# Kernel optimization log

Measured on AMD Instinct MI355X. Metric: run time of the kernel, lower is better.

Reference implementation:

```python
import jax, jax.numpy as jnp
import numpy as np

B, L, D, H = 2, 4096, 768, 12
Dh = D // H


def setup_inputs() -> dict:
    key = jax.random.key(0)
    k1, k2, k3 = jax.random.split(key, 3)
    x = jax.random.normal(k1, (B, L, D), dtype=jnp.float32)
    Wqkv = jax.random.normal(k2, (D, 3 * D), dtype=jnp.float32) * 0.02
    bqkv = jnp.zeros((3 * D,), dtype=jnp.float32)
    Wo = jax.random.normal(k3, (D, D), dtype=jnp.float32) * 0.02
    bo = jnp.zeros((D,), dtype=jnp.float32)
    return {"x": x, "Wqkv": Wqkv, "bqkv": bqkv, "Wo": Wo, "bo": bo}


def reference(x, Wqkv, bqkv, Wo, bo):
    Bs, Ls, Ds = x.shape
    # fused QKV projection
    qkv = x @ Wqkv + bqkv  # [B, L, 3D]
    q, k, v = jnp.split(qkv, 3, axis=2)
    q = q.reshape(Bs, Ls, H, Dh)
    k = k.reshape(Bs, Ls, H, Dh)
    v = v.reshape(Bs, Ls, H, Dh)
    # scaled dot-product attention with causal mask (fp32 softmax, as flax dpa with dtype=float32)
    scale = 1.0 / np.sqrt(Dh)
    scores = jnp.einsum('bqhd,bkhd->bhqk', q, k) * scale  # [B, H, L, L]
    causal = jnp.tril(jnp.ones((Ls, Ls), dtype=bool))
    big_neg = jnp.finfo(jnp.float32).min
    scores = jnp.where(causal[None, None, :, :], scores, big_neg)
    attn = jax.nn.softmax(scores, axis=-1)
    y = jnp.einsum('bhqk,bkhd->bqhd', attn, v)  # [B, L, H, Dh]
    y = y.reshape(Bs, Ls, Ds)
    # output projection
    return y @ Wo + bo
```

## Files before the change

kernel.cpp:

```cpp
#include <hip/hip_runtime.h>
#include <hip/hip_bf16.h>
#include <stdint.h>

#define BB 2
#define LL 4096
#define DD 768
#define HH 12
#define DH 64
#define MM (BB * LL)
#define NQKV (3 * DD)
#define KK 768
#define PLANE ((size_t)BB * HH * LL * DH)
#define SQSCALE 0.1803368801111204f

typedef __attribute__((ext_vector_type(8))) short bf16x8;
typedef __attribute__((ext_vector_type(4))) float f32x4;

__device__ __forceinline__ float bf2f(uint16_t u) {
  union { uint32_t u; float f; } c; c.u = ((uint32_t)u) << 16; return c.f;
}
__device__ __forceinline__ uint16_t f2bf(float f) {
  union { float f; uint32_t u; } c; c.f = f;
  return (uint16_t)((c.u + 0x7FFFu + ((c.u >> 16) & 1u)) >> 16);
}
__device__ __forceinline__ uint32_t cvt2(float a, float b) {
  __hip_bfloat162 h = __float22bfloat162_rn(make_float2(a, b));
  union { __hip_bfloat162 h; uint32_t u; } c; c.h = h; return c.u;
}

union H8 { uint16_t h[8]; uint32_t w[4]; uint4 v; };
union B8 { uint2 d[2]; bf16x8 v; };

template <bool F32>
__device__ __forceinline__ H8 load8(const void* p, size_t idx) {
  H8 r;
  if (F32) {
    const float* f = (const float*)p + idx;
    float4 a = *(const float4*)f;
    float4 b = *(const float4*)(f + 4);
    r.w[0] = cvt2(a.x, a.y); r.w[1] = cvt2(a.z, a.w);
    r.w[2] = cvt2(b.x, b.y); r.w[3] = cvt2(b.z, b.w);
  } else {
    r.v = *(const uint4*)((const uint16_t*)p + idx);
  }
  return r;
}

__device__ __forceinline__ void g2l16(const uint16_t* g, uint16_t* l) {
  __builtin_amdgcn_global_load_lds((const __attribute__((address_space(1))) void*)g,
                                   (__attribute__((address_space(3))) void*)l,
                                   16, 0, 0);
}

__global__ void detect_k(const uint16_t* __restrict__ x, int* __restrict__ flag) {
  __shared__ int cnt;
  if (threadIdx.x == 0) cnt = 0;
  __syncthreads();
  int c = 0;
  for (int i = threadIdx.x; i < 4096; i += 256) {
    int e = (x[i] >> 7) & 0xFF;
    if (e == 0xFF || e > 133 || e < 100) c++;
  }
  atomicAdd(&cnt, c);
  __syncthreads();
  if (threadIdx.x == 0) *flag = (cnt > 512) ? 1 : 0;
}

__global__ __launch_bounds__(256) void prep_k(const void* __restrict__ x,
                                              uint16_t* __restrict__ xbf,
                                              const void* __restrict__ Wqkv,
                                              uint16_t* __restrict__ wqkvT,
                                              const void* __restrict__ Wo,
                                              uint16_t* __restrict__ woT,
                                              const int* __restrict__ flag) {
  __shared__ uint16_t Ts[64][65];
  const int fl = *flag;
  const int id = blockIdx.x;
  const int tid = threadIdx.x;
  if (id < 768) {
    size_t base = (size_t)id * 1024 + tid;
#pragma unroll
    for (int j = 0; j < 4; ++j) {
      size_t i = base + j * 256;
      H8 v = fl ? load8<true>(x, i * 8) : load8<false>(x, i * 8);
      *(uint4*)(xbf + i * 8) = v.v;
    }
    return;
  }
  const void* W;
  uint16_t* WT;
  int N, widx;
  if (id < 1200) { W = Wqkv; WT = wqkvT; N = NQKV; widx = id - 768; }
  else           { W = Wo;   WT = woT;   N = DD;   widx = id - 1200; }
  const int nb = N / 64;
  const int n0 = (widx % nb) * 64, k0 = (widx / nb) * 64;
#pragma unroll
  for (int j = 0; j < 16; ++j) {
    int idx = tid + j * 256;
    int r = idx >> 6, c = idx & 63;
    size_t gi = (size_t)(k0 + r) * N + n0 + c;
    float v = fl ? ((const float*)W)[gi] : bf2f(((const uint16_t*)W)[gi]);
    Ts[c][r] = f2bf(v);
  }
  __syncthreads();
#pragma unroll
  for (int j = 0; j < 16; ++j) {
    int idx = tid + j * 256;
    int n = idx >> 6, k = idx & 63;
    WT[(size_t)(n0 + n) * KK + k0 + k] = Ts[n][k];
  }
}

__device__ __forceinline__ void gemm128_core(const uint16_t* __restrict__ A,
                                             const uint16_t* __restrict__ BT,
                                             int m0, int n0,
                                             uint16_t* As, uint16_t* Bs,
                                             f32x4 acc[4][4]) {
  const int tid = threadIdx.x, lane = tid & 63, w = tid >> 6;
  const int quad = lane >> 4, c16 = lane & 15;
  const int wm = w >> 1, wn = w & 1;
  const int srow = lane >> 2, schunk = lane & 3;
  const int rsw = (c16 >> 1) & 3;
  for (int k0 = 0; k0 < KK; k0 += 32) {
#pragma unroll
    for (int i = 0; i < 2; ++i) {
      int row = w * 32 + i * 16 + srow;
      int gch = schunk ^ ((row >> 1) & 3);
      g2l16(A + (size_t)(m0 + row) * KK + k0 + gch * 8, As + (w * 32 + i * 16) * 32);
      g2l16(BT + (size_t)(n0 + row) * KK + k0 + gch * 8, Bs + (w * 32 + i * 16) * 32);
    }
    __syncthreads();
    bf16x8 a[4], b[4];
#pragma unroll
    for (int i = 0; i < 4; ++i) {
      a[i] = *(const bf16x8*)(As + (wm * 64 + i * 16 + c16) * 32 + ((quad ^ rsw) * 8));
      b[i] = *(const bf16x8*)(Bs + (wn * 64 + i * 16 + c16) * 32 + ((quad ^ rsw) * 8));
    }
#pragma unroll
    for (int i = 0; i < 4; ++i)
#pragma unroll
      for (int f = 0; f < 4; ++f)
        acc[i][f] = __builtin_amdgcn_mfma_f32_16x16x32_bf16(a[i], b[f], acc[i][f], 0, 0, 0);
    __syncthreads();
  }
}

__global__ __launch_bounds__(256) void qkv128_k(const uint16_t* __restrict__ X,
                                                const uint16_t* __restrict__ WT,
                                                const void* __restrict__ bias,
                                                uint16_t* __restrict__ planes,
                                                const int* __restrict__ flag) {
  __shared__ __align__(16) uint16_t smem[8704];
  uint16_t* As = smem;
  uint16_t* Bs = smem + 4096;
  const int fl = *flag;
  const int m0 = blockIdx.x * 128, n0 = blockIdx.y * 128;
  f32x4 acc[4][4];
#pragma unroll
  for (int i = 0; i < 4; ++i)
#pragma unroll
    for (int f = 0; f < 4; ++f) acc[i][f] = (f32x4){0.f, 0.f, 0.f, 0.f};
  gemm128_core(X, WT, m0, n0, As, Bs, acc);

  const int tid = threadIdx.x, lane = tid & 63, w = tid >> 6;
  const int quad = lane >> 4, c16 = lane & 15;
  const int wm = w >> 1, wn = w & 1;
  const int which = (n0 >= 2 * DD) ? 2 : (n0 >= DD ? 1 : 0);

  if (which < 2) {
    uint16_t* dst = planes + (size_t)which * PLANE;
    const float sc = (which == 0) ? SQSCALE : 1.0f;
#pragma unroll
    for (int f = 0; f < 4; ++f) {
      int n = n0 + wn * 64 + f * 16 + c16;
      float bv = fl ? ((const float*)bias)[n] : bf2f(((const uint16_t*)bias)[n]);
      int rem = n - which * DD;
      int hh = rem >> 6, dd = rem & 63;
#pragma unroll
      for (int i = 0; i < 4; ++i) {
        uint32_t pa = cvt2((acc[i][f][0] + bv) * sc, (acc[i][f][1] + bv) * sc);
        uint32_t pb = cvt2((acc[i][f][2] + bv) * sc, (acc[i][f][3] + bv) * sc);
        int m = m0 + wm * 64 + i * 16 + quad * 4;
        int b = m >> 12, l = m & (LL - 1);
        uint16_t* base = dst + ((size_t)(b * HH + hh) * LL + l) * DH + dd;
        base[0 * DH] = (uint16_t)pa;
        base[1 * DH] = (uint16_t)(pa >> 16);
        base[2 * DH] = (uint16_t)pb;
        base[3 * DH] = (uint16_t)(pb >> 16);
      }
    }
  } else {
    uint16_t (*Ts)[136] = reinterpret_cast<uint16_t(*)[136]>(smem);
    uint16_t* vtp = planes + 2 * PLANE;
    const int l0 = m0 & (LL - 1), bb = m0 >> 12;
    for (int half = 0; half < 2; ++half) {
      __syncthreads();
      if (wn == half) {
#pragma unroll
        for (int f = 0; f < 4; ++f) {
          int n = n0 + half * 64 + f * 16 + c16;
          float bv = fl ? ((const float*)bias)[n] : bf2f(((const uint16_t*)bias)[n]);
#pragma unroll
          for (int i = 0; i < 4; ++i) {
            uint32_t pa = cvt2(acc[i][f][0] + bv, acc[i][f][1] + bv);
            uint32_t pb = cvt2(acc[i][f][2] + bv, acc[i][f][3] + bv);
            *(uint2*)(&Ts[f * 16 + c16][wm * 64 + i * 16 + quad * 4]) = make_uint2(pa, pb);
          }
        }
      }
      __syncthreads();
#pragma unroll
      for (int j = 0; j < 4; ++j) {
        int idx = tid + j * 256;
        int nl = idx >> 4, ch = idx & 15;
        int rem = n0 + half * 64 + nl - 2 * DD;
        int hh = rem >> 6, dd = rem & 63;
        uint4 val = *(const uint4*)(&Ts[nl][ch * 8]);
        *(uint4*)(vtp + ((size_t)(bb * HH + hh) * DH + dd) * LL + l0 + ch * 8) = val;
      }
    }
  }
}

__global__ __launch_bounds__(256) void attn_k(const uint16_t* __restrict__ planes,
                                              uint16_t* __restrict__ y) {
  __shared__ __align__(16) uint16_t Ks[2][64 * 64];
  __shared__ __align__(16) uint16_t Vt[2][64 * 64];
  __shared__ __align__(16) uint16_t Ps[4][16 * 64];
  const int p = blockIdx.x;
  const int bh = blockIdx.y;
  const uint16_t* qb = planes + (size_t)bh * LL * DH;
  const uint16_t* kb = qb + PLANE;
  const uint16_t* vtb = planes + 2 * PLANE + (size_t)bh * DH * LL;
  const int tid = threadIdx.x, lane = tid & 63, wv = tid >> 6;
  const int quad = lane >> 4, c16 = lane & 15;
  const int r0 = tid >> 3, c0 = tid & 7;
  const int sw0 = r0 & 7;
  const int swf = c16 & 7;
  uint16_t* Psb = Ps[wv];
  const int b = bh / HH, hh = bh - b * HH;
  const int pwbase = c16 * 64;
  const int prd0 = pwbase + (((2 * quad) ^ c16) << 2);
  const int prd1 = pwbase + (((2 * quad + 1) ^ c16) << 2);
  const int prd2 = pwbase + (((8 + 2 * quad) ^ c16) << 2);
  const int prd3 = pwbase + (((8 + 2 * quad + 1) ^ c16) << 2);

  for (int pass = 0; pass < 2; ++pass) {
    const int qi = pass ? p : 63 - p;
    const int q0 = qi * 64;
    const size_t qoff = (size_t)(q0 + wv * 16 + c16) * DH;
    bf16x8 qf0 = *(const bf16x8*)(qb + qoff + quad * 8);
    bf16x8 qf1 = *(const bf16x8*)(qb + qoff + 32 + quad * 8);

    f32x4 o[4];
#pragma unroll
    for (int g = 0; g < 4; ++g) o[g] = (f32x4){0.f, 0.f, 0.f, 0.f};
    float l_i = 0.f;

    uint4 kr0 = *(const uint4*)(kb + (size_t)r0 * DH + c0 * 8);
    uint4 kr1 = *(const uint4*)(kb + (size_t)(r0 + 32) * DH + c0 * 8);
    uint4 vr0 = *(const uint4*)(vtb + (size_t)r0 * LL + c0 * 8);
    uint4 vr1 = *(const uint4*)(vtb + (size_t)(r0 + 32) * LL + c0 * 8);

    for (int t = 0; t <= qi; ++t) {
      uint16_t* kd = Ks[t & 1];
      uint16_t* vd = Vt[t & 1];
      *(uint4*)(kd + r0 * 64 + (c0 ^ sw0) * 8) = kr0;
      *(uint4*)(kd + (r0 + 32) * 64 + (c0 ^ sw0) * 8) = kr1;
      *(uint4*)(vd + r0 * 64 + (c0 ^ sw0) * 8) = vr0;
      *(uint4*)(vd + (r0 + 32) * 64 + (c0 ^ sw0) * 8) = vr1;
      if (t < qi) {
        int t64 = (t + 1) * 64;
        kr0 = *(const uint4*)(kb + (size_t)(t64 + r0) * DH + c0 * 8);
        kr1 = *(const uint4*)(kb + (size_t)(t64 + r0 + 32) * DH + c0 * 8);
        vr0 = *(const uint4*)(vtb + (size_t)r0 * LL + t64 + c0 * 8);
        vr1 = *(const uint4*)(vtb + (size_t)(r0 + 32) * LL + t64 + c0 * 8);
      }
      __syncthreads();

      f32x4 s[4];
#pragma unroll
      for (int f = 0; f < 4; ++f) {
        const uint16_t* krow = kd + (f * 16 + c16) * 64;
        bf16x8 k0f = *(const bf16x8*)(krow + ((quad ^ swf) * 8));
        bf16x8 k1f = *(const bf16x8*)(krow + (((quad + 4) ^ swf) * 8));
        f32x4 z = {0.f, 0.f, 0.f, 0.f};
        z = __builtin_amdgcn_mfma_f32_16x16x32_bf16(k0f, qf0, z, 0, 0, 0);
        z = __builtin_amdgcn_mfma_f32_16x16x32_bf16(k1f, qf1, z, 0, 0, 0);
        s[f] = z;
      }
      const int qg = q0 + wv * 16 + c16;
      if (t == qi) {
#pragma unroll
        for (int f = 0; f < 4; ++f) {
          int key0 = t * 64 + f * 16 + quad * 4;
#pragma unroll
          for (int r = 0; r < 4; ++r) {
            float pv = exp2f(s[f][r]);
            pv = (key0 + r <= qg) ? pv : 0.f;
            s[f][r] = pv;
            l_i += pv;
          }
        }
      } else {
#pragma unroll
        for (int f = 0; f < 4; ++f)
#pragma unroll
          for (int r = 0; r < 4; ++r) {
            float pv = exp2f(s[f][r]);
            s[f][r] = pv;
            l_i += pv;
          }
      }
#pragma unroll
      for (int f = 0; f < 4; ++f) {
        uint32_t w0 = cvt2(s[f][0], s[f][1]);
        uint32_t w1 = cvt2(s[f][2], s[f][3]);
        *(uint2*)(Psb + pwbase + (((f * 4 + quad) ^ c16) << 2)) = make_uint2(w0, w1);
      }
      __asm__ __volatile__("s_waitcnt lgkmcnt(0)" ::: "memory");
      B8 p0, p1;
      p0.d[0] = *(const uint2*)(Psb + prd0);
      p0.d[1] = *(const uint2*)(Psb + prd1);
      p1.d[0] = *(const uint2*)(Psb + prd2);
      p1.d[1] = *(const uint2*)(Psb + prd3);
#pragma unroll
      for (int g = 0; g < 4; ++g) {
        const uint16_t* vrow = vd + (g * 16 + c16) * 64;
        bf16x8 v0 = *(const bf16x8*)(vrow + ((quad ^ swf) * 8));
        bf16x8 v1 = *(const bf16x8*)(vrow + (((quad + 4) ^ swf) * 8));
        o[g] = __builtin_amdgcn_mfma_f32_16x16x32_bf16(p0.v, v0, o[g], 0, 0, 0);
        o[g] = __builtin_amdgcn_mfma_f32_16x16x32_bf16(p1.v, v1, o[g], 0, 0, 0);
      }
    }

    l_i += __shfl_xor(l_i, 16);
    l_i += __shfl_xor(l_i, 32);
    float inv[4];
#pragma unroll
    for (int r = 0; r < 4; ++r)
      inv[r] = 1.f / __shfl(l_i, (quad << 4) + quad * 4 + r);
#pragma unroll
    for (int g = 0; g < 4; ++g) {
      uint32_t pa = cvt2(o[g][0] * inv[0], o[g][1] * inv[1]);
      uint32_t pb = cvt2(o[g][2] * inv[2], o[g][3] * inv[3]);
      int l = q0 + wv * 16 + quad * 4;
      uint16_t* base = y + ((size_t)(b * LL + l)) * DD + hh * DH + g * 16 + c16;
      base[0 * DD] = (uint16_t)pa;
      base[1 * DD] = (uint16_t)(pa >> 16);
      base[2 * DD] = (uint16_t)pb;
      base[3 * DD] = (uint16_t)(pb >> 16);
    }
    __syncthreads();
  }
}

__global__ __launch_bounds__(256) void out64_k(const uint16_t* __restrict__ Y,
                                               const uint16_t* __restrict__ WT,
                                               const void* __restrict__ bias,
                                               void* __restrict__ out,
                                               const int* __restrict__ flag) {
  __shared__ __align__(16) uint16_t As[128 * 32];
  __shared__ __align__(16) uint16_t Bs[64 * 32];
  const int fl = *flag;
  const int m0 = blockIdx.x * 128, n0 = blockIdx.y * 64;
  const int tid = threadIdx.x, lane = tid & 63, w = tid >> 6;
  const int quad = lane >> 4, c16 = lane & 15;
  const int srow = lane >> 2, schunk = lane & 3;
  const int rsw = (c16 >> 1) & 3;
  f32x4 acc[2][4];
#pragma unroll
  for (int i = 0; i < 2; ++i)
#pragma unroll
    for (int f = 0; f < 4; ++f) acc[i][f] = (f32x4){0.f, 0.f, 0.f, 0.f};
  for (int k0 = 0; k0 < KK; k0 += 32) {
#pragma unroll
    for (int i = 0; i < 2; ++i) {
      int row = w * 32 + i * 16 + srow;
      int gch = schunk ^ ((row >> 1) & 3);
      g2l16(Y + (size_t)(m0 + row) * KK + k0 + gch * 8, As + (w * 32 + i * 16) * 32);
    }
    {
      int row = w * 16 + srow;
      int gch = schunk ^ ((row >> 1) & 3);
      g2l16(WT + (size_t)(n0 + row) * KK + k0 + gch * 8, Bs + (w * 16) * 32);
    }
    __syncthreads();
    bf16x8 a[2], bfr[4];
#pragma unroll
    for (int i = 0; i < 2; ++i)
      a[i] = *(const bf16x8*)(As + (w * 32 + i * 16 + c16) * 32 + ((quad ^ rsw) * 8));
#pragma unroll
    for (int f = 0; f < 4; ++f)
      bfr[f] = *(const bf16x8*)(Bs + (f * 16 + c16) * 32 + ((quad ^ rsw) * 8));
#pragma unroll
    for (int i = 0; i < 2; ++i)
#pragma unroll
      for (int f = 0; f < 4; ++f)
        acc[i][f] = __builtin_amdgcn_mfma_f32_16x16x32_bf16(a[i], bfr[f], acc[i][f], 0, 0, 0);
    __syncthreads();
  }
#pragma unroll
  for (int f = 0; f < 4; ++f) {
    int n = n0 + f * 16 + c16;
    float bv = fl ? ((const float*)bias)[n] : bf2f(((const uint16_t*)bias)[n]);
#pragma unroll
    for (int i = 0; i < 2; ++i) {
      int m = m0 + w * 32 + i * 16 + quad * 4;
      if (fl) {
        float* base = (float*)out + (size_t)m * DD + n;
#pragma unroll
        for (int r = 0; r < 4; ++r) base[r * DD] = acc[i][f][r] + bv;
      } else {
        uint32_t pa = cvt2(acc[i][f][0] + bv, acc[i][f][1] + bv);
        uint32_t pb = cvt2(acc[i][f][2] + bv, acc[i][f][3] + bv);
        uint16_t* base = (uint16_t*)out + (size_t)m * DD + n;
        base[0 * DD] = (uint16_t)pa;
        base[1 * DD] = (uint16_t)(pa >> 16);
        base[2 * DD] = (uint16_t)pb;
        base[3 * DD] = (uint16_t)(pb >> 16);
      }
    }
  }
}

extern "C" void kernel_launch(void* const* d_in, const int* in_sizes, int n_in,
                              void* d_out, int out_size, void* d_ws, size_t ws_size,
                              hipStream_t stream) {
  const void* x    = d_in[0];
  const void* Wqkv = d_in[1];
  const void* bqkv = d_in[2];
  const void* Wo   = d_in[3];
  const void* bo   = d_in[4];
  int* flagp = (int*)d_ws;
  uint16_t* planes = (uint16_t*)((char*)d_ws + 64);
  uint16_t* y_ws   = planes + 3 * PLANE;
  uint16_t* wqkvT  = y_ws + (size_t)MM * DD;
  uint16_t* woT    = wqkvT + (size_t)NQKV * KK;
  uint16_t* xbf    = y_ws;

  detect_k<<<1, 256, 0, stream>>>((const uint16_t*)x, flagp);
  prep_k<<<1344, 256, 0, stream>>>(x, xbf, Wqkv, wqkvT, Wo, woT, flagp);
  qkv128_k<<<dim3(MM / 128, NQKV / 128), 256, 0, stream>>>(xbf, wqkvT, bqkv, planes, flagp);
  attn_k<<<dim3(32, BB * HH), 256, 0, stream>>>(planes, y_ws);
  out64_k<<<dim3(MM / 128, DD / 64), 256, 0, stream>>>(y_ws, woT, bo, d_out, flagp);
}
```

Baseline: 272.4 us.

## Feed P from registers via permuted V layout and launch one q-tile per block

```diff
diff --git a/kernel.cpp b/kernel.cpp
--- a/kernel.cpp
+++ b/kernel.cpp
@@ -226,8 +226,7 @@
                                               uint16_t* __restrict__ y) {
   __shared__ __align__(16) uint16_t Ks[2][64 * 64];
   __shared__ __align__(16) uint16_t Vt[2][64 * 64];
-  __shared__ __align__(16) uint16_t Ps[4][16 * 64];
-  const int p = blockIdx.x;
+  const int qi = 63 - blockIdx.x;
   const int bh = blockIdx.y;
   const uint16_t* qb = planes + (size_t)bh * LL * DH;
   const uint16_t* kb = qb + PLANE;
@@ -237,121 +236,122 @@
   const int r0 = tid >> 3, c0 = tid & 7;
   const int sw0 = r0 & 7;
   const int swf = c16 & 7;
-  uint16_t* Psb = Ps[wv];
   const int b = bh / HH, hh = bh - b * HH;
-  const int pwbase = c16 * 64;
-  const int prd0 = pwbase + (((2 * quad) ^ c16) << 2);
-  const int prd1 = pwbase + (((2 * quad + 1) ^ c16) << 2);
-  const int prd2 = pwbase + (((8 + 2 * quad) ^ c16) << 2);
-  const int prd3 = pwbase + (((8 + 2 * quad + 1) ^ c16) << 2);
-
-  for (int pass = 0; pass < 2; ++pass) {
-    const int qi = pass ? p : 63 - p;
-    const int q0 = qi * 64;
-    const size_t qoff = (size_t)(q0 + wv * 16 + c16) * DH;
-    bf16x8 qf0 = *(const bf16x8*)(qb + qoff + quad * 8);
-    bf16x8 qf1 = *(const bf16x8*)(qb + qoff + 32 + quad * 8);
-
-    f32x4 o[4];
-#pragma unroll
-    for (int g = 0; g < 4; ++g) o[g] = (f32x4){0.f, 0.f, 0.f, 0.f};
-    float l_i = 0.f;
-
-    uint4 kr0 = *(const uint4*)(kb + (size_t)r0 * DH + c0 * 8);
-    uint4 kr1 = *(const uint4*)(kb + (size_t)(r0 + 32) * DH + c0 * 8);
-    uint4 vr0 = *(const uint4*)(vtb + (size_t)r0 * LL + c0 * 8);
-    uint4 vr1 = *(const uint4*)(vtb + (size_t)(r0 + 32) * LL + c0 * 8);
-
-    for (int t = 0; t <= qi; ++t) {
-      uint16_t* kd = Ks[t & 1];
-      uint16_t* vd = Vt[t & 1];
-      *(uint4*)(kd + r0 * 64 + (c0 ^ sw0) * 8) = kr0;
-      *(uint4*)(kd + (r0 + 32) * 64 + (c0 ^ sw0) * 8) = kr1;
-      *(uint4*)(vd + r0 * 64 + (c0 ^ sw0) * 8) = vr0;
-      *(uint4*)(vd + (r0 + 32) * 64 + (c0 ^ sw0) * 8) = vr1;
-      if (t < qi) {
-        int t64 = (t + 1) * 64;
-        kr0 = *(const uint4*)(kb + (size_t)(t64 + r0) * DH + c0 * 8);
-        kr1 = *(const uint4*)(kb + (size_t)(t64 + r0 + 32) * DH + c0 * 8);
-        vr0 = *(const uint4*)(vtb + (size_t)r0 * LL + t64 + c0 * 8);
-        vr1 = *(const uint4*)(vtb + (size_t)(r0 + 32) * LL + t64 + c0 * 8);
+
+  const int kw0 = r0 * 64 + (c0 ^ sw0) * 8;
+  const int kw1 = (r0 + 32) * 64 + (c0 ^ sw0) * 8;
+  int vw0, vw1, vw2, vw3;
+  {
+    int ksA = 8 * c0;
+    int ksB = 8 * c0 + 4;
+    int chA = ((ksA & 32) >> 3) + ((ksA >> 2) & 3);
+    int chB = ((ksB & 32) >> 3) + ((ksB >> 2) & 3);
+    int fA = ((ksA >> 4) & 1) * 4;
+    int fB = ((ksB >> 4) & 1) * 4;
+    vw0 = r0 * 64 + ((chA ^ sw0) * 8) + fA;
+    vw1 = r0 * 64 + ((chB ^ sw0) * 8) + fB;
+    vw2 = (r0 + 32) * 64 + ((chA ^ sw0) * 8) + fA;
+    vw3 = (r0 + 32) * 64 + ((chB ^ sw0) * 8) + fB;
+  }
+
+  const int q0 = qi * 64;
+  const size_t qoff = (size_t)(q0 + wv * 16 + c16) * DH;
+  bf16x8 qf0 = *(const bf16x8*)(qb + qoff + quad * 8);
+  bf16x8 qf1 = *(const bf16x8*)(qb + qoff + 32 + quad * 8);
+
+  f32x4 o[4];
+#pragma unroll
+  for (int g = 0; g < 4; ++g) o[g] = (f32x4){0.f, 0.f, 0.f, 0.f};
+  float l_i = 0.f;
+
+  uint4 kr0 = *(const uint4*)(kb + (size_t)r0 * DH + c0 * 8);
+  uint4 kr1 = *(const uint4*)(kb + (size_t)(r0 + 32) * DH + c0 * 8);
+  uint4 vr0 = *(const uint4*)(vtb + (size_t)r0 * LL + c0 * 8);
+  uint4 vr1 = *(const uint4*)(vtb + (size_t)(r0 + 32) * LL + c0 * 8);
+
+  for (int t = 0; t <= qi; ++t) {
+    uint16_t* kd = Ks[t & 1];
+    uint16_t* vd = Vt[t & 1];
+    *(uint4*)(kd + kw0) = kr0;
+    *(uint4*)(kd + kw1) = kr1;
+    *(uint2*)(vd + vw0) = make_uint2(vr0.x, vr0.y);
+    *(uint2*)(vd + vw1) = make_uint2(vr0.z, vr0.w);
+    *(uint2*)(vd + vw2) = make_uint2(vr1.x, vr1.y);
+    *(uint2*)(vd + vw3) = make_uint2(vr1.z, vr1.w);
+    if (t < qi) {
+      int t64 = (t + 1) * 64;
+      kr0 = *(const uint4*)(kb + (size_t)(t64 + r0) * DH + c0 * 8);
+      kr1 = *(const uint4*)(kb + (size_t)(t64 + r0 + 32) * DH + c0 * 8);
+      vr0 = *(const uint4*)(vtb + (size_t)r0 * LL + t64 + c0 * 8);
+      vr1 = *(const uint4*)(vtb + (size_t)(r0 + 32) * LL + t64 + c0 * 8);
+    }
+    __syncthreads();
+
+    f32x4 s[4];
+#pragma unroll
+    for (int f = 0; f < 4; ++f) {
+      const uint16_t* krow = kd + (f * 16 + c16) * 64;
+      bf16x8 k0f = *(const bf16x8*)(krow + ((quad ^ swf) * 8));
+      bf16x8 k1f = *(const bf16x8*)(krow + (((quad + 4) ^ swf) * 8));
+      f32x4 z = {0.f, 0.f, 0.f, 0.f};
+      z = __builtin_amdgcn_mfma_f32_16x16x32_bf16(k0f, qf0, z, 0, 0, 0);
+      z = __builtin_amdgcn_mfma_f32_16x16x32_bf16(k1f, qf1, z, 0, 0, 0);
+      s[f] = z;
+    }
+    const int qg = q0 + wv * 16 + c16;
+    if (t == qi) {
+#pragma unroll
+      for (int f = 0; f < 4; ++f) {
+        int key0 = t * 64 + f * 16 + quad * 4;
+#pragma unroll
+        for (int r = 0; r < 4; ++r) {
+          float pv = exp2f(s[f][r]);
+          pv = (key0 + r <= qg) ? pv : 0.f;
+          s[f][r] = pv;
+          l_i += pv;
+        }
       }
-      __syncthreads();
-
-      f32x4 s[4];
-#pragma unroll
-      for (int f = 0; f < 4; ++f) {
-        const uint16_t* krow = kd + (f * 16 + c16) * 64;
-        bf16x8 k0f = *(const bf16x8*)(krow + ((quad ^ swf) * 8));
-        bf16x8 k1f = *(const bf16x8*)(krow + (((quad + 4) ^ swf) * 8));
-        f32x4 z = {0.f, 0.f, 0.f, 0.f};
-        z = __builtin_amdgcn_mfma_f32_16x16x32_bf16(k0f, qf0, z, 0, 0, 0);
-        z = __builtin_amdgcn_mfma_f32_16x16x32_bf16(k1f, qf1, z, 0, 0, 0);
-        s[f] = z;
-      }
-      const int qg = q0 + wv * 16 + c16;
-      if (t == qi) {
-#pragma unroll
-        for (int f = 0; f < 4; ++f) {
-          int key0 = t * 64 + f * 16 + quad * 4;
-#pragma unroll
-          for (int r = 0; r < 4; ++r) {
-            float pv = exp2f(s[f][r]);
-            pv = (key0 + r <= qg) ? pv : 0.f;
-            s[f][r] = pv;
-            l_i += pv;
-          }
+    } else {
+#pragma unroll
+      for (int f = 0; f < 4; ++f)
+#pragma unroll
+        for (int r = 0; r < 4; ++r) {
+          float pv = exp2f(s[f][r]);
+          s[f][r] = pv;
+          l_i += pv;
         }
-      } else {
-#pragma unroll
-        for (int f = 0; f < 4; ++f)
-#pragma unroll
-          for (int r = 0; r < 4; ++r) {
-            float pv = exp2f(s[f][r]);
-            s[f][r] = pv;
-            l_i += pv;
-          }
-      }
-#pragma unroll
-      for (int f = 0; f < 4; ++f) {
-        uint32_t w0 = cvt2(s[f][0], s[f][1]);
-        uint32_t w1 = cvt2(s[f][2], s[f][3]);
-        *(uint2*)(Psb + pwbase + (((f * 4 + quad) ^ c16) << 2)) = make_uint2(w0, w1);
-      }
-      __asm__ __volatile__("s_waitcnt lgkmcnt(0)" ::: "memory");
-      B8 p0, p1;
-      p0.d[0] = *(const uint2*)(Psb + prd0);
-      p0.d[1] = *(const uint2*)(Psb + prd1);
-      p1.d[0] = *(const uint2*)(Psb + prd2);
-      p1.d[1] = *(const uint2*)(Psb + prd3);
-#pragma unroll
-      for (int g = 0; g < 4; ++g) {
-        const uint16_t* vrow = vd + (g * 16 + c16) * 64;
-        bf16x8 v0 = *(const bf16x8*)(vrow + ((quad ^ swf) * 8));
-        bf16x8 v1 = *(const bf16x8*)(vrow + (((quad + 4) ^ swf) * 8));
-        o[g] = __builtin_amdgcn_mfma_f32_16x16x32_bf16(p0.v, v0, o[g], 0, 0, 0);
-        o[g] = __builtin_amdgcn_mfma_f32_16x16x32_bf16(p1.v, v1, o[g], 0, 0, 0);
-      }
-    }
-
-    l_i += __shfl_xor(l_i, 16);
-    l_i += __shfl_xor(l_i, 32);
-    float inv[4];
-#pragma unroll
-    for (int r = 0; r < 4; ++r)
-      inv[r] = 1.f / __shfl(l_i, (quad << 4) + quad * 4 + r);
+    }
+    B8 p0, p1;
+    p0.d[0] = make_uint2(cvt2(s[0][0], s[0][1]), cvt2(s[0][2], s[0][3]));
+    p0.d[1] = make_uint2(cvt2(s[1][0], s[1][1]), cvt2(s[1][2], s[1][3]));
+    p1.d[0] = make_uint2(cvt2(s[2][0], s[2][1]), cvt2(s[2][2], s[2][3]));
+    p1.d[1] = make_uint2(cvt2(s[3][0], s[3][1]), cvt2(s[3][2], s[3][3]));
 #pragma unroll
     for (int g = 0; g < 4; ++g) {
-      uint32_t pa = cvt2(o[g][0] * inv[0], o[g][1] * inv[1]);
-      uint32_t pb = cvt2(o[g][2] * inv[2], o[g][3] * inv[3]);
-      int l = q0 + wv * 16 + quad * 4;
-      uint16_t* base = y + ((size_t)(b * LL + l)) * DD + hh * DH + g * 16 + c16;
-      base[0 * DD] = (uint16_t)pa;
-      base[1 * DD] = (uint16_t)(pa >> 16);
-      base[2 * DD] = (uint16_t)pb;
-      base[3 * DD] = (uint16_t)(pb >> 16);
-    }
-    __syncthreads();
+      const uint16_t* vrow = vd + (g * 16 + c16) * 64;
+      bf16x8 v0 = *(const bf16x8*)(vrow + ((quad ^ swf) * 8));
+      bf16x8 v1 = *(const bf16x8*)(vrow + (((quad + 4) ^ swf) * 8));
+      o[g] = __builtin_amdgcn_mfma_f32_16x16x32_bf16(p0.v, v0, o[g], 0, 0, 0);
+      o[g] = __builtin_amdgcn_mfma_f32_16x16x32_bf16(p1.v, v1, o[g], 0, 0, 0);
+    }
+  }
+
+  l_i += __shfl_xor(l_i, 16);
+  l_i += __shfl_xor(l_i, 32);
+  float inv[4];
+#pragma unroll
+  for (int r = 0; r < 4; ++r)
+    inv[r] = 1.f / __shfl(l_i, (quad << 4) + quad * 4 + r);
+#pragma unroll
+  for (int g = 0; g < 4; ++g) {
+    uint32_t pa = cvt2(o[g][0] * inv[0], o[g][1] * inv[1]);
+    uint32_t pb = cvt2(o[g][2] * inv[2], o[g][3] * inv[3]);
+    int l = q0 + wv * 16 + quad * 4;
+    uint16_t* base = y + ((size_t)(b * LL + l)) * DD + hh * DH + g * 16 + c16;
+    base[0 * DD] = (uint16_t)pa;
+    base[1 * DD] = (uint16_t)(pa >> 16);
+    base[2 * DD] = (uint16_t)pb;
+    base[3 * DD] = (uint16_t)(pb >> 16);
   }
 }
 
@@ -442,6 +442,6 @@
   detect_k<<<1, 256, 0, stream>>>((const uint16_t*)x, flagp);
   prep_k<<<1344, 256, 0, stream>>>(x, xbf, Wqkv, wqkvT, Wo, woT, flagp);
   qkv128_k<<<dim3(MM / 128, NQKV / 128), 256, 0, stream>>>(xbf, wqkvT, bqkv, planes, flagp);
-  attn_k<<<dim3(32, BB * HH), 256, 0, stream>>>(planes, y_ws);
+  attn_k<<<dim3(64, BB * HH), 256, 0, stream>>>(planes, y_ws);
   out64_k<<<dim3(MM / 128, DD / 64), 256, 0, stream>>>(y_ws, woT, bo, d_out, flagp);
 }
```

New measurement: 312.2 us. +14.6%, slower.

## Feed softmax probs straight from registers into PV MFMA using 128-key tiles

Applied to the files above, without the earlier changes.

```diff
diff --git a/kernel.cpp b/kernel.cpp
--- a/kernel.cpp
+++ b/kernel.cpp
@@ -224,9 +224,8 @@
 
 __global__ __launch_bounds__(256) void attn_k(const uint16_t* __restrict__ planes,
                                               uint16_t* __restrict__ y) {
-  __shared__ __align__(16) uint16_t Ks[2][64 * 64];
-  __shared__ __align__(16) uint16_t Vt[2][64 * 64];
-  __shared__ __align__(16) uint16_t Ps[4][16 * 64];
+  __shared__ __align__(16) uint16_t Ks[128 * 64];
+  __shared__ __align__(16) uint16_t Vt[64 * 128];
   const int p = blockIdx.x;
   const int bh = blockIdx.y;
   const uint16_t* qb = planes + (size_t)bh * LL * DH;
@@ -234,54 +233,79 @@
   const uint16_t* vtb = planes + 2 * PLANE + (size_t)bh * DH * LL;
   const int tid = threadIdx.x, lane = tid & 63, wv = tid >> 6;
   const int quad = lane >> 4, c16 = lane & 15;
-  const int r0 = tid >> 3, c0 = tid & 7;
-  const int sw0 = r0 & 7;
   const int swf = c16 & 7;
-  uint16_t* Psb = Ps[wv];
   const int b = bh / HH, hh = bh - b * HH;
-  const int pwbase = c16 * 64;
-  const int prd0 = pwbase + (((2 * quad) ^ c16) << 2);
-  const int prd1 = pwbase + (((2 * quad + 1) ^ c16) << 2);
-  const int prd2 = pwbase + (((8 + 2 * quad) ^ c16) << 2);
-  const int prd3 = pwbase + (((8 + 2 * quad + 1) ^ c16) << 2);
+
+  const int kr = tid >> 3, kc = tid & 7;
+  int kwoff[4];
+#pragma unroll
+  for (int j = 0; j < 4; ++j) {
+    int row = 4 * kr + j;
+    kwoff[j] = row * 64 + ((kc ^ (row & 7)) * 8);
+  }
+  const int dr = tid >> 2, kg = tid & 3;
+  const int swd = dr & 7;
+  int vwoff[4][2];
+#pragma unroll
+  for (int j = 0; j < 4; ++j) {
+#pragma unroll
+    for (int h = 0; h < 2; ++h) {
+      int ks = (kg + 4 * j) * 8 + h * 4;
+      int G = ks >> 6, ks6 = ks & 63;
+      int ch = ((ks6 & 32) >> 3) + ((ks6 >> 2) & 3);
+      int f4 = ((ks6 >> 4) & 1) * 4;
+      vwoff[j][h] = dr * 128 + G * 64 + ((ch ^ swd ^ (G << 2)) * 8) + f4;
+    }
+  }
+
+  B8 ones;
+  ones.d[0] = make_uint2(0x3F803F80u, 0x3F803F80u);
+  ones.d[1] = make_uint2(0x3F803F80u, 0x3F803F80u);
 
   for (int pass = 0; pass < 2; ++pass) {
     const int qi = pass ? p : 63 - p;
+    const int nt = (qi + 2) >> 1;
     const int q0 = qi * 64;
     const size_t qoff = (size_t)(q0 + wv * 16 + c16) * DH;
     bf16x8 qf0 = *(const bf16x8*)(qb + qoff + quad * 8);
     bf16x8 qf1 = *(const bf16x8*)(qb + qoff + 32 + quad * 8);
 
-    f32x4 o[4];
+    f32x4 o[4], lacc = (f32x4){0.f, 0.f, 0.f, 0.f};
 #pragma unroll
     for (int g = 0; g < 4; ++g) o[g] = (f32x4){0.f, 0.f, 0.f, 0.f};
-    float l_i = 0.f;
-
-    uint4 kr0 = *(const uint4*)(kb + (size_t)r0 * DH + c0 * 8);
-    uint4 kr1 = *(const uint4*)(kb + (size_t)(r0 + 32) * DH + c0 * 8);
-    uint4 vr0 = *(const uint4*)(vtb + (size_t)r0 * LL + c0 * 8);
-    uint4 vr1 = *(const uint4*)(vtb + (size_t)(r0 + 32) * LL + c0 * 8);
-
-    for (int t = 0; t <= qi; ++t) {
-      uint16_t* kd = Ks[t & 1];
-      uint16_t* vd = Vt[t & 1];
-      *(uint4*)(kd + r0 * 64 + (c0 ^ sw0) * 8) = kr0;
-      *(uint4*)(kd + (r0 + 32) * 64 + (c0 ^ sw0) * 8) = kr1;
-      *(uint4*)(vd + r0 * 64 + (c0 ^ sw0) * 8) = vr0;
-      *(uint4*)(vd + (r0 + 32) * 64 + (c0 ^ sw0) * 8) = vr1;
-      if (t < qi) {
-        int t64 = (t + 1) * 64;
-        kr0 = *(const uint4*)(kb + (size_t)(t64 + r0) * DH + c0 * 8);
-        kr1 = *(const uint4*)(kb + (size_t)(t64 + r0 + 32) * DH + c0 * 8);
-        vr0 = *(const uint4*)(vtb + (size_t)r0 * LL + t64 + c0 * 8);
-        vr1 = *(const uint4*)(vtb + (size_t)(r0 + 32) * LL + t64 + c0 * 8);
-      }
+
+    const uint16_t* kp = kb + (size_t)(4 * kr) * DH + kc * 8;
+    const uint16_t* vp = vtb + (size_t)dr * LL + kg * 8;
+    uint4 krg[4], vrg[4];
+#pragma unroll
+    for (int j = 0; j < 4; ++j) {
+      krg[j] = *(const uint4*)(kp + j * DH);
+      vrg[j] = *(const uint4*)(vp + j * 32);
+    }
+    kp += 128 * DH; vp += 128;
+
+    for (int t = 0; t < nt; ++t) {
       __syncthreads();
-
-      f32x4 s[4];
-#pragma unroll
-      for (int f = 0; f < 4; ++f) {
-        const uint16_t* krow = kd + (f * 16 + c16) * 64;
+#pragma unroll
+      for (int j = 0; j < 4; ++j) {
+        *(uint4*)(Ks + kwoff[j]) = krg[j];
+        *(uint2*)(Vt + vwoff[j][0]) = make_uint2(vrg[j].x, vrg[j].y);
+        *(uint2*)(Vt + vwoff[j][1]) = make_uint2(vrg[j].z, vrg[j].w);
+      }
+      if (t + 1 < nt) {
+#pragma unroll
+        for (int j = 0; j < 4; ++j) {
+          krg[j] = *(const uint4*)(kp + j * DH);
+          vrg[j] = *(const uint4*)(vp + j * 32);
+        }
+        kp += 128 * DH; vp += 128;
+      }
+      __syncthreads();
+
+      f32x4 s[8];
+#pragma unroll
+      for (int f = 0; f < 8; ++f) {
+        const uint16_t* krow = Ks + (f * 16 + c16) * 64;
         bf16x8 k0f = *(const bf16x8*)(krow + ((quad ^ swf) * 8));
         bf16x8 k1f = *(const bf16x8*)(krow + (((quad + 4) ^ swf) * 8));
         f32x4 z = {0.f, 0.f, 0.f, 0.f};
@@ -290,56 +314,49 @@
         s[f] = z;
       }
       const int qg = q0 + wv * 16 + c16;
-      if (t == qi) {
-#pragma unroll
-        for (int f = 0; f < 4; ++f) {
-          int key0 = t * 64 + f * 16 + quad * 4;
+      if (t == nt - 1) {
+#pragma unroll
+        for (int f = 0; f < 8; ++f) {
+          int key0 = t * 128 + f * 16 + quad * 4;
 #pragma unroll
           for (int r = 0; r < 4; ++r) {
             float pv = exp2f(s[f][r]);
-            pv = (key0 + r <= qg) ? pv : 0.f;
-            s[f][r] = pv;
-            l_i += pv;
+            s[f][r] = (key0 + r <= qg) ? pv : 0.f;
           }
         }
       } else {
 #pragma unroll
-        for (int f = 0; f < 4; ++f)
-#pragma unroll
-          for (int r = 0; r < 4; ++r) {
-            float pv = exp2f(s[f][r]);
-            s[f][r] = pv;
-            l_i += pv;
-          }
-      }
-#pragma unroll
-      for (int f = 0; f < 4; ++f) {
-        uint32_t w0 = cvt2(s[f][0], s[f][1]);
-        uint32_t w1 = cvt2(s[f][2], s[f][3]);
-        *(uint2*)(Psb + pwbase + (((f * 4 + quad) ^ c16) << 2)) = make_uint2(w0, w1);
-      }
-      __asm__ __volatile__("s_waitcnt lgkmcnt(0)" ::: "memory");
-      B8 p0, p1;
-      p0.d[0] = *(const uint2*)(Psb + prd0);
-      p0.d[1] = *(const uint2*)(Psb + prd1);
-      p1.d[0] = *(const uint2*)(Psb + prd2);
-      p1.d[1] = *(const uint2*)(Psb + prd3);
+        for (int f = 0; f < 8; ++f)
+#pragma unroll
+          for (int r = 0; r < 4; ++r) s[f][r] = exp2f(s[f][r]);
+      }
+      B8 pk[4];
+#pragma unroll
+      for (int h = 0; h < 4; ++h) {
+        pk[h].d[0] = make_uint2(cvt2(s[2 * h][0], s[2 * h][1]),
+                                cvt2(s[2 * h][2], s[2 * h][3]));
+        pk[h].d[1] = make_uint2(cvt2(s[2 * h + 1][0], s[2 * h + 1][1]),
+                                cvt2(s[2 * h + 1][2], s[2 * h + 1][3]));
+      }
+#pragma unroll
+      for (int h = 0; h < 4; ++h)
+        lacc = __builtin_amdgcn_mfma_f32_16x16x32_bf16(pk[h].v, ones.v, lacc, 0, 0, 0);
 #pragma unroll
       for (int g = 0; g < 4; ++g) {
-        const uint16_t* vrow = vd + (g * 16 + c16) * 64;
-        bf16x8 v0 = *(const bf16x8*)(vrow + ((quad ^ swf) * 8));
-        bf16x8 v1 = *(const bf16x8*)(vrow + (((quad + 4) ^ swf) * 8));
-        o[g] = __builtin_amdgcn_mfma_f32_16x16x32_bf16(p0.v, v0, o[g], 0, 0, 0);
-        o[g] = __builtin_amdgcn_mfma_f32_16x16x32_bf16(p1.v, v1, o[g], 0, 0, 0);
-      }
-    }
-
-    l_i += __shfl_xor(l_i, 16);
-    l_i += __shfl_xor(l_i, 32);
+        const uint16_t* vrow = Vt + (g * 16 + c16) * 128;
+#pragma unroll
+        for (int sl = 0; sl < 4; ++sl) {
+          int G = sl >> 1;
+          int chunk = (quad + 4 * (sl & 1)) ^ swf ^ (G << 2);
+          bf16x8 vv = *(const bf16x8*)(vrow + G * 64 + chunk * 8);
+          o[g] = __builtin_amdgcn_mfma_f32_16x16x32_bf16(pk[sl].v, vv, o[g], 0, 0, 0);
+        }
+      }
+    }
+
     float inv[4];
 #pragma unroll
-    for (int r = 0; r < 4; ++r)
-      inv[r] = 1.f / __shfl(l_i, (quad << 4) + quad * 4 + r);
+    for (int r = 0; r < 4; ++r) inv[r] = 1.f / lacc[r];
 #pragma unroll
     for (int g = 0; g < 4; ++g) {
       uint32_t pa = cvt2(o[g][0] * inv[0], o[g][1] * inv[1]);
@@ -351,7 +368,6 @@
       base[2 * DD] = (uint16_t)pb;
       base[3 * DD] = (uint16_t)(pb >> 16);
     }
-    __syncthreads();
   }
 }
 
```

Result: slower. 347.0 us (+27.4%).
